# Performance work log

Measured on AMD Instinct MI355X. Metric: run time of the kernel, lower is better.

## Reference

```python
import jax, jax.numpy as jnp
import numpy as np

B, T, M, P = 256, 256, 512, 512


def setup_inputs() -> dict:
    key = jax.random.key(0)
    ks = jax.random.split(key, 10)
    sc = lambda fan: 1.0 / np.sqrt(fan)
    return {
        "H": jax.random.normal(ks[0], (B, T, M), jnp.float32),
        "d0": jax.random.normal(ks[1], (1, B, P), jnp.float32),
        "s0": jax.random.normal(ks[2], (1, B, P), jnp.float32),
        # TemporalAttention params (torch Linear convention: y = x @ W.T)
        "W_d": jax.random.uniform(ks[3], (M, 2 * P), jnp.float32, -sc(2 * P), sc(2 * P)),
        "U_d": jax.random.uniform(ks[4], (M, M), jnp.float32, -sc(M), sc(M)),
        "v_d": jax.random.uniform(ks[5], (1, M), jnp.float32, -sc(M), sc(M)),
        # LSTM params (torch nn.LSTM convention, gate order i,f,g,o)
        "W_ih": jax.random.uniform(ks[6], (4 * P, M), jnp.float32, -sc(P), sc(P)),
        "W_hh": jax.random.uniform(ks[7], (4 * P, P), jnp.float32, -sc(P), sc(P)),
        "b_ih": jax.random.uniform(ks[8], (4 * P,), jnp.float32, -sc(P), sc(P)),
        "b_hh": jax.random.uniform(ks[9], (4 * P,), jnp.float32, -sc(P), sc(P)),
    }


def reference(H, d0, s0, W_d, U_d, v_d, W_ih, W_hh, b_ih, b_hh):
    T_steps = H.shape[1]
    # U_d(H) is time-invariant across decode steps: precompute once. [B,T,m]
    UH = jnp.einsum("btm,nm->btn", H, U_d)
    v = v_d[0]  # [m]

    def step(carry, _):
        d, s = carry  # [B,p] hidden, [B,p] cell
        q = jnp.concatenate([d, s], axis=-1)            # [B,2p]
        wq = q @ W_d.T                                   # [B,m]
        e = jnp.tanh(wq[:, None, :] + UH) @ v            # [B,T]
        beta = jax.nn.softmax(e, axis=1)                 # softmax over time
        c_t = jnp.einsum("bt,btm->bm", beta, H)          # [B,m]
        gates = c_t @ W_ih.T + b_ih + d @ W_hh.T + b_hh  # [B,4p]
        i, f, g, o = jnp.split(gates, 4, axis=-1)
        s_new = jax.nn.sigmoid(f) * s + jax.nn.sigmoid(i) * jnp.tanh(g)
        d_new = jax.nn.sigmoid(o) * jnp.tanh(s_new)
        return (d_new, s_new), (beta, c_t)

    (d, s), (betas, cts) = jax.lax.scan(step, (d0[0], s0[0]), None, length=T_steps)
    attn = jnp.transpose(betas, (1, 0, 2))               # [B,T,T]
    out = jnp.concatenate([d[:, None, :], cts[-1][:, None, :]], axis=2)  # [B,1,p+m]
    return out, attn
```

## Files before the change

kernel.cpp:

```cpp
#include <hip/hip_runtime.h>
#include <hip/hip_fp16.h>

typedef _Float16 h4 __attribute__((ext_vector_type(4)));
typedef _Float16 h8 __attribute__((ext_vector_type(8)));
typedef float    f4 __attribute__((ext_vector_type(4)));

#define SC2LOG2E 2.8853900817779268f

__device__ __forceinline__ float v_exp2(float x) { float r; asm("v_exp_f32 %0, %1" : "=v"(r) : "v"(x)); return r; }
__device__ __forceinline__ float v_rcp (float x) { float r; asm("v_rcp_f32 %0, %1" : "=v"(r) : "v"(x)); return r; }
__device__ __forceinline__ float fast_tanh(float x) {
    float e = __expf(2.0f * x);
    return 1.0f - 2.0f * v_rcp(e + 1.0f);
}
__device__ __forceinline__ float fast_sigmoid(float x) {
    return v_rcp(1.0f + __expf(-x));
}

__device__ __forceinline__ h8 ld_h8_dc(const _Float16* p) {
    h8 r;
    asm volatile("global_load_dwordx4 %0, %1, off sc0 sc1" : "=v"(r) : "v"(p));
    return r;
}
__device__ __forceinline__ f4 ld_f4_dc(const float* p) {
    f4 r;
    asm volatile("global_load_dwordx4 %0, %1, off sc0 sc1" : "=v"(r) : "v"(p));
    return r;
}
__device__ __forceinline__ void st_f_dc(float* p, float v) {
    asm volatile("global_store_dword %0, %1, off sc0 sc1" :: "v"(p), "v"(v) : "memory");
}
__device__ __forceinline__ void st_h_dc(_Float16* p, _Float16 v) {
    unsigned u = (unsigned)__builtin_bit_cast(unsigned short, v);
    asm volatile("global_store_short %0, %1, off sc0 sc1" :: "v"(p), "v"(u) : "memory");
}

__global__ void convert_f16(const float* __restrict__ s, _Float16* __restrict__ d, int n) {
    int i = (blockIdx.x * 256 + threadIdx.x) * 4;
    if (i < n) {
        float4 v = *(const float4*)(s + i);
        h4 o = {(_Float16)v.x, (_Float16)v.y, (_Float16)v.z, (_Float16)v.w};
        *(h4*)(d + i) = o;
    }
}

__global__ void convert_cb(const float* __restrict__ H, _Float16* __restrict__ CB) {
    int i = (blockIdx.x * 256 + threadIdx.x) * 4;
    int r = i >> 9, m = i & 511;
    float4 v = *(const float4*)(H + i);
    h4 o = {(_Float16)v.x, (_Float16)v.y, (_Float16)v.z, (_Float16)v.w};
    *(h4*)(CB + (size_t)r * 1024 + 512 + m) = o;
}

__global__ void build_wg(const float* __restrict__ Wih, const float* __restrict__ Whh,
                         _Float16* __restrict__ Wg) {
    int idx = (blockIdx.x * 256 + threadIdx.x) * 4;
    int np = idx >> 10, k = idx & 1023;
    int p = np >> 2, g = np & 3, row = g * 512 + p;
    const float* src = (k < 512) ? Wih + (size_t)row * 512 + k
                                 : Whh + (size_t)row * 512 + (k - 512);
    float4 v = *(const float4*)src;
    h4 o = {(_Float16)v.x, (_Float16)v.y, (_Float16)v.z, (_Float16)v.w};
    *(h4*)(Wg + idx) = o;
}

__global__ void build_bsum(const float* __restrict__ bih, const float* __restrict__ bhh,
                           float* __restrict__ bsum) {
    int np = blockIdx.x * 256 + threadIdx.x;
    int p = np >> 2, g = np & 3, row = g * 512 + p;
    bsum[np] = bih[row] + bhh[row];
}

__global__ void init_state(const float* __restrict__ d0, const float* __restrict__ s0,
                           _Float16* __restrict__ qA, _Float16* __restrict__ ds) {
    int i = blockIdx.x * 256 + threadIdx.x;
    float dv = d0[i], sv = s0[i];
    int b = i >> 9, j = i & 511;
    qA[(size_t)b * 1024 + 512 + j] = (_Float16)dv;
    ds[(size_t)b * 1024 + j]       = (_Float16)dv;
    ds[(size_t)b * 1024 + 512 + j] = (_Float16)sv;
}

__global__ void zero_bar(unsigned* __restrict__ bar, int n) {
    int i = blockIdx.x * 256 + threadIdx.x;
    if (i < n) bar[i] = 0u;
}

__global__ __launch_bounds__(128) void uh_mfma(const float* __restrict__ H,
                                               const float* __restrict__ Ud,
                                               _Float16* __restrict__ CB) {
    int tid = threadIdx.x;
    int lane = tid & 63, w = tid >> 6;
    int ln = lane & 15, quad = lane >> 4;
    int m0 = blockIdx.x * 64, n0 = blockIdx.y * 32;
    f4 z = {0.f, 0.f, 0.f, 0.f};
    f4 acc[4] = {z, z, z, z};
    const float* brow = Ud + (size_t)(n0 + w * 16 + ln) * 512 + quad * 8;
    const float* arow = H  + (size_t)(m0 + ln) * 512 + quad * 8;
#pragma unroll 2
    for (int k = 0; k < 16; k++) {
        float4 bx = *(const float4*)(brow + k * 32);
        float4 by = *(const float4*)(brow + k * 32 + 4);
        h8 b = {(_Float16)bx.x, (_Float16)bx.y, (_Float16)bx.z, (_Float16)bx.w,
                (_Float16)by.x, (_Float16)by.y, (_Float16)by.z, (_Float16)by.w};
#pragma unroll
        for (int mt = 0; mt < 4; mt++) {
            const float* ap = arow + (size_t)mt * 16 * 512 + k * 32;
            float4 ax = *(const float4*)ap;
            float4 ay = *(const float4*)(ap + 4);
            h8 a = {(_Float16)ax.x, (_Float16)ax.y, (_Float16)ax.z, (_Float16)ax.w,
                    (_Float16)ay.x, (_Float16)ay.y, (_Float16)ay.z, (_Float16)ay.w};
            acc[mt] = __builtin_amdgcn_mfma_f32_16x16x32_f16(a, b, acc[mt], 0, 0, 0);
        }
    }
#pragma unroll
    for (int mt = 0; mt < 4; mt++)
#pragma unroll
        for (int r = 0; r < 4; r++)
            CB[(size_t)(m0 + mt * 16 + quad * 4 + r) * 1024 + n0 + w * 16 + ln] =
                (_Float16)(acc[mt][r] * SC2LOG2E);
}

__device__ __forceinline__ void gbar(unsigned* __restrict__ arrive,
                                     unsigned* __restrict__ gen,
                                     unsigned ticket) {
    __syncthreads();
    if (blockIdx.x == 0) {
        int tid = threadIdx.x;
        if (tid >= 1 && tid < 256) {
            while (__hip_atomic_load(arrive + (size_t)tid * 16, __ATOMIC_RELAXED,
                                     __HIP_MEMORY_SCOPE_AGENT) < ticket)
                __builtin_amdgcn_s_sleep(2);
        }
        __syncthreads();
        if (tid == 0)
            __hip_atomic_store(gen, ticket, __ATOMIC_RELAXED, __HIP_MEMORY_SCOPE_AGENT);
    } else {
        if (threadIdx.x == 0) {
            __hip_atomic_store(arrive + (size_t)blockIdx.x * 16, ticket,
                               __ATOMIC_RELAXED, __HIP_MEMORY_SCOPE_AGENT);
            while (__hip_atomic_load(gen, __ATOMIC_RELAXED,
                                     __HIP_MEMORY_SCOPE_AGENT) < ticket)
                __builtin_amdgcn_s_sleep(2);
        }
        __syncthreads();
    }
}

struct LoopArgs {
    const _Float16* CB;
    const _Float16* Wdh;
    const _Float16* Wg;
    const float*    bsum;
    const float*    vd;
    const float*    s0;
    float*          wq2;
    _Float16*       qA;
    _Float16*       qB;
    _Float16*       ds;
    float*          out;
    float*          attn;
    unsigned*       bar;
};

__global__ __launch_bounds__(1024) void decoder_loop(LoopArgs A) {
    const int bid = blockIdx.x;
    const int tid = threadIdx.x;
    const int lane = tid & 63, wv = tid >> 6;
    const int ln = lane & 15, quad = lane >> 4;

    __shared__ __align__(16) union {
        struct { float cpart[16][512]; float es2[256]; float m2s[16]; float zs[16]; } B;
        float gt[64][36];
    } sm;

    unsigned* arrive = A.bar;
    unsigned* gen    = A.bar + 4096;
    unsigned  bt     = 0;

    const int a_m0 = (bid >> 5) * 64, a_n0 = (bid & 31) * 16;
    const float4* vp = (const float4*)(A.vd + lane * 8);
    float4 vv0 = vp[0], vv1 = vp[1];
    float vr[8] = {vv0.x, vv0.y, vv0.z, vv0.w, vv1.x, vv1.y, vv1.z, vv1.w};
    const h8* ub0 = (const h8*)(A.CB + ((size_t)bid * 256 + wv * 16) * 1024) + lane;
    const int c_mt = wv & 3, c_nt = (wv >> 2) & 1;
    const int c_m0 = (bid & 3) * 64, c_by = bid >> 2;
    const int c_n0 = c_by * 32, c_p0 = c_by * 8;
    const float c_bs = A.bsum[c_n0 + c_nt * 16 + ln];
    const int c_ml = tid >> 3, c_pl = tid & 7;
    const int c_b = c_m0 + c_ml, c_p = c_p0 + c_pl;
    float s_state = (tid < 512) ? A.s0[(size_t)c_b * 512 + c_p] : 0.f;

#pragma unroll 1
    for (int t = 0; t < 256; ++t) {
        _Float16* qcur = (t & 1) ? A.qB : A.qA;
        _Float16* qnxt = (t & 1) ? A.qA : A.qB;

        if (bid < 128 && tid < 256) {
            f4 acc = {0.f, 0.f, 0.f, 0.f};
            const h8* ap = (const h8*)(A.ds  + (size_t)(a_m0 + wv * 16 + ln) * 1024) + quad;
            const h8* bp = (const h8*)(A.Wdh + (size_t)(a_n0 + ln) * 1024) + quad;
#pragma unroll
            for (int kc = 0; kc < 4; ++kc) {
                h8 areg[8];
#pragma unroll
                for (int u = 0; u < 8; ++u)
                    areg[u] = ld_h8_dc((const _Float16*)(ap + (kc * 8 + u) * 4));
                asm volatile("s_waitcnt vmcnt(0)" ::: "memory");
                __builtin_amdgcn_sched_barrier(0);
#pragma unroll
                for (int u = 0; u < 8; ++u)
                    acc = __builtin_amdgcn_mfma_f32_16x16x32_f16(areg[u], bp[(kc * 8 + u) * 4],
                                                                 acc, 0, 0, 0);
            }
#pragma unroll
            for (int r = 0; r < 4; ++r)
                st_f_dc(A.wq2 + (size_t)(a_m0 + wv * 16 + quad * 4 + r) * 512 + a_n0 + ln,
                        acc[r] * SC2LOG2E);
        }
        gbar(arrive, gen, ++bt);

        {
            f4 w0 = ld_f4_dc(A.wq2 + (size_t)bid * 512 + lane * 8);
            f4 w1 = ld_f4_dc(A.wq2 + (size_t)bid * 512 + lane * 8 + 4);
            asm volatile("s_waitcnt vmcnt(0)" ::: "memory");
            __builtin_amdgcn_sched_barrier(0);
            float wr[8] = {w0[0], w0[1], w0[2], w0[3], w1[0], w1[1], w1[2], w1[3]};

            float m2 = -1e30f, Z = 0.f;
            float ch[8] = {0.f, 0.f, 0.f, 0.f, 0.f, 0.f, 0.f, 0.f};
#pragma unroll 4
            for (int i = 0; i < 16; ++i) {
                h8 u  = ub0[(size_t)i * 128];
                h8 hv = ub0[(size_t)i * 128 + 64];
                float acc = 0.0f;
#pragma unroll
                for (int j = 0; j < 8; ++j) {
                    float zz = wr[j] + (float)u[j];
                    acc = fmaf(vr[j], v_rcp(1.0f + v_exp2(zz)), acc);
                }
#pragma unroll
                for (int o = 32; o; o >>= 1) acc += __shfl_xor(acc, o, 64);
                float e2 = -SC2LOG2E * acc;
                if (lane == 0) sm.B.es2[wv * 16 + i] = e2;
                if (e2 > m2) {
                    float s = v_exp2(m2 - e2);
                    Z *= s;
#pragma unroll
                    for (int k2 = 0; k2 < 8; ++k2) ch[k2] *= s;
                    m2 = e2;
                }
                float w = v_exp2(e2 - m2);
                Z += w;
#pragma unroll
                for (int k2 = 0; k2 < 8; ++k2) ch[k2] = fmaf(w, (float)hv[k2], ch[k2]);
            }
            *(float4*)&sm.B.cpart[wv][lane * 8]     = make_float4(ch[0], ch[1], ch[2], ch[3]);
            *(float4*)&sm.B.cpart[wv][lane * 8 + 4] = make_float4(ch[4], ch[5], ch[6], ch[7]);
            if (lane == 0) { sm.B.m2s[wv] = m2; sm.B.zs[wv] = Z; }
            __syncthreads();

            if (tid < 512) {
                float m2g = sm.B.m2s[0];
#pragma unroll
                for (int w2 = 1; w2 < 16; ++w2) m2g = fmaxf(m2g, sm.B.m2s[w2]);
                float Zg = 0.f, cg = 0.f;
#pragma unroll
                for (int w2 = 0; w2 < 16; ++w2) {
                    float f = v_exp2(sm.B.m2s[w2] - m2g);
                    Zg = fmaf(sm.B.zs[w2], f, Zg);
                    cg = fmaf(sm.B.cpart[w2][tid], f, cg);
                }
                float rz = v_rcp(Zg);
                float cval = cg * rz;
                st_h_dc(qcur + (size_t)bid * 1024 + tid, (_Float16)cval);
                if (t == 255) A.out[(size_t)bid * 1024 + 512 + tid] = cval;
                if (tid < 256) {
                    float beta = v_exp2(sm.B.es2[tid] - m2g) * rz;
                    __builtin_nontemporal_store(beta,
                        A.attn + (size_t)bid * 65536 + (size_t)t * 256 + tid);
                }
            }
        }
        gbar(arrive, gen, ++bt);

        {
            bool act = (tid < 512);
            if (act) {
                f4 acc = {0.f, 0.f, 0.f, 0.f};
                const h8* ap = (const h8*)(qcur + (size_t)(c_m0 + c_mt * 16 + ln) * 1024) + quad;
                const h8* bp = (const h8*)(A.Wg + (size_t)(c_n0 + c_nt * 16 + ln) * 1024) + quad;
#pragma unroll
                for (int kc = 0; kc < 4; ++kc) {
                    h8 areg[8];
#pragma unroll
                    for (int u = 0; u < 8; ++u)
                        areg[u] = ld_h8_dc((const _Float16*)(ap + (kc * 8 + u) * 4));
                    asm volatile("s_waitcnt vmcnt(0)" ::: "memory");
                    __builtin_amdgcn_sched_barrier(0);
#pragma unroll
                    for (int u = 0; u < 8; ++u)
                        acc = __builtin_amdgcn_mfma_f32_16x16x32_f16(areg[u], bp[(kc * 8 + u) * 4],
                                                                     acc, 0, 0, 0);
                }
#pragma unroll
                for (int r = 0; r < 4; ++r)
                    sm.gt[c_mt * 16 + quad * 4 + r][c_nt * 16 + ln] = acc[r] + c_bs;
            }
            __syncthreads();
            if (act) {
                float4 g4 = *(const float4*)&sm.gt[c_ml][c_pl * 4];
                float ig = fast_sigmoid(g4.x);
                float fg = fast_sigmoid(g4.y);
                float gg = fast_tanh(g4.z);
                float og = fast_sigmoid(g4.w);
                float snew = fmaf(fg, s_state, ig * gg);
                float dnew = og * fast_tanh(snew);
                s_state = snew;
                st_h_dc(qnxt + (size_t)c_b * 1024 + 512 + c_p, (_Float16)dnew);
                st_h_dc(A.ds + (size_t)c_b * 1024 + c_p,       (_Float16)dnew);
                st_h_dc(A.ds + (size_t)c_b * 1024 + 512 + c_p, (_Float16)snew);
                if (t == 255) A.out[(size_t)c_b * 1024 + c_p] = dnew;
            }
        }
        gbar(arrive, gen, ++bt);
    }
}

extern "C" void kernel_launch(void* const* d_in, const int* in_sizes, int n_in,
                              void* d_out, int out_size, void* d_ws, size_t ws_size,
                              hipStream_t stream) {
    const float* H   = (const float*)d_in[0];
    const float* d0  = (const float*)d_in[1];
    const float* s0  = (const float*)d_in[2];
    const float* Wd  = (const float*)d_in[3];
    const float* Ud  = (const float*)d_in[4];
    const float* vd  = (const float*)d_in[5];
    const float* Wih = (const float*)d_in[6];
    const float* Whh = (const float*)d_in[7];
    const float* bih = (const float*)d_in[8];
    const float* bhh = (const float*)d_in[9];

    float* out  = (float*)d_out;
    float* attn = out + 262144;

    char* ws = (char*)d_ws;
    size_t off = 0;
    _Float16* CB   = (_Float16*)(ws + off); off += 134217728;
    _Float16* Wdh  = (_Float16*)(ws + off); off += 1048576;
    _Float16* Wg   = (_Float16*)(ws + off); off += 4194304;
    float*    bsum = (float*)   (ws + off); off += 8192;
    float*    wq2  = (float*)   (ws + off); off += 524288;
    _Float16* qA   = (_Float16*)(ws + off); off += 524288;
    _Float16* qB   = (_Float16*)(ws + off); off += 524288;
    _Float16* ds   = (_Float16*)(ws + off); off += 524288;
    unsigned* bar  = (unsigned*)(ws + off); off += 32768;

    convert_f16<<<512, 256, 0, stream>>>(Wd, Wdh, 524288);
    build_wg<<<2048, 256, 0, stream>>>(Wih, Whh, Wg);
    build_bsum<<<8, 256, 0, stream>>>(bih, bhh, bsum);
    convert_cb<<<32768, 256, 0, stream>>>(H, CB);
    init_state<<<512, 256, 0, stream>>>(d0, s0, qA, ds);
    zero_bar<<<17, 256, 0, stream>>>(bar, 4097);
    uh_mfma<<<dim3(1024, 16), 128, 0, stream>>>(H, Ud, CB);

    LoopArgs la;
    la.CB = CB; la.Wdh = Wdh; la.Wg = Wg; la.bsum = bsum; la.vd = vd; la.s0 = s0;
    la.wq2 = wq2; la.qA = qA; la.qB = qB; la.ds = ds;
    la.out = out; la.attn = attn; la.bar = bar;
    void* kp[] = { &la };
    if (hipLaunchCooperativeKernel((void*)decoder_loop, dim3(256), dim3(1024),
                                   kp, 0, stream) != hipSuccess) {
        decoder_loop<<<dim3(256), dim3(1024), 0, stream>>>(la);
    }
}
```

Measured before the change: 16.22 ms.

## Halve decoder block size and prefetch attention UH/H rows across the barrier

Shrinks the persistent decoder kernel from 1024 to 512 threads per block, so each wave handles 32 time rows instead of 16. At the start of each step it issues register prefetches of the block's UH and H rows before the wq GEMM and grid barrier, then walks them with staged vmcnt waits, reissuing loads for the second half. The goal is to hide the global-memory latency of the attention scan behind the earlier phase and barrier, and to remove the idle half of the block in the gate phase. The cost is heavy register pressure from 32 held h8 vectors, which may cause spills, and fewer waves available to hide latency.

```diff
diff --git a/kernel.cpp b/kernel.cpp
--- a/kernel.cpp
+++ b/kernel.cpp
@@ -33,6 +33,31 @@
 __device__ __forceinline__ void st_h_dc(_Float16* p, _Float16 v) {
     unsigned u = (unsigned)__builtin_bit_cast(unsigned short, v);
     asm volatile("global_store_short %0, %1, off sc0 sc1" :: "v"(p), "v"(u) : "memory");
+}
+__device__ __forceinline__ h8 ld_h8(const _Float16* p) {
+    h8 r;
+    asm volatile("global_load_dwordx4 %0, %1, off" : "=v"(r) : "v"(p));
+    return r;
+}
+__device__ __forceinline__ void wait_vmcnt(int n) {
+    switch (n) {
+    case 0:  asm volatile("s_waitcnt vmcnt(0)"  ::: "memory"); break;
+    case 2:  asm volatile("s_waitcnt vmcnt(2)"  ::: "memory"); break;
+    case 4:  asm volatile("s_waitcnt vmcnt(4)"  ::: "memory"); break;
+    case 6:  asm volatile("s_waitcnt vmcnt(6)"  ::: "memory"); break;
+    case 8:  asm volatile("s_waitcnt vmcnt(8)"  ::: "memory"); break;
+    case 10: asm volatile("s_waitcnt vmcnt(10)" ::: "memory"); break;
+    case 12: asm volatile("s_waitcnt vmcnt(12)" ::: "memory"); break;
+    case 14: asm volatile("s_waitcnt vmcnt(14)" ::: "memory"); break;
+    case 16: asm volatile("s_waitcnt vmcnt(16)" ::: "memory"); break;
+    case 18: asm volatile("s_waitcnt vmcnt(18)" ::: "memory"); break;
+    case 20: asm volatile("s_waitcnt vmcnt(20)" ::: "memory"); break;
+    case 22: asm volatile("s_waitcnt vmcnt(22)" ::: "memory"); break;
+    case 24: asm volatile("s_waitcnt vmcnt(24)" ::: "memory"); break;
+    case 26: asm volatile("s_waitcnt vmcnt(26)" ::: "memory"); break;
+    case 28: asm volatile("s_waitcnt vmcnt(28)" ::: "memory"); break;
+    default: asm volatile("s_waitcnt vmcnt(30)" ::: "memory"); break;
+    }
 }
 
 __global__ void convert_f16(const float* __restrict__ s, _Float16* __restrict__ d, int n) {
@@ -163,14 +188,14 @@
     unsigned*       bar;
 };
 
-__global__ __launch_bounds__(1024) void decoder_loop(LoopArgs A) {
+__global__ __launch_bounds__(512, 2) void decoder_loop(LoopArgs A) {
     const int bid = blockIdx.x;
     const int tid = threadIdx.x;
     const int lane = tid & 63, wv = tid >> 6;
     const int ln = lane & 15, quad = lane >> 4;
 
     __shared__ __align__(16) union {
-        struct { float cpart[16][512]; float es2[256]; float m2s[16]; float zs[16]; } B;
+        struct { float cpart[8][512]; float es2[256]; float m2s[8]; float zs[8]; } B;
         float gt[64][36];
     } sm;
 
@@ -182,19 +207,26 @@
     const float4* vp = (const float4*)(A.vd + lane * 8);
     float4 vv0 = vp[0], vv1 = vp[1];
     float vr[8] = {vv0.x, vv0.y, vv0.z, vv0.w, vv1.x, vv1.y, vv1.z, vv1.w};
-    const h8* ub0 = (const h8*)(A.CB + ((size_t)bid * 256 + wv * 16) * 1024) + lane;
+    const _Float16* cb0 = A.CB + ((size_t)bid * 256 + wv * 32) * 1024 + lane * 8;
     const int c_mt = wv & 3, c_nt = (wv >> 2) & 1;
     const int c_m0 = (bid & 3) * 64, c_by = bid >> 2;
     const int c_n0 = c_by * 32, c_p0 = c_by * 8;
     const float c_bs = A.bsum[c_n0 + c_nt * 16 + ln];
     const int c_ml = tid >> 3, c_pl = tid & 7;
     const int c_b = c_m0 + c_ml, c_p = c_p0 + c_pl;
-    float s_state = (tid < 512) ? A.s0[(size_t)c_b * 512 + c_p] : 0.f;
+    float s_state = A.s0[(size_t)c_b * 512 + c_p];
 
 #pragma unroll 1
     for (int t = 0; t < 256; ++t) {
         _Float16* qcur = (t & 1) ? A.qB : A.qA;
         _Float16* qnxt = (t & 1) ? A.qA : A.qB;
+
+        h8 su[16], sh[16];
+#pragma unroll
+        for (int r = 0; r < 16; ++r) {
+            su[r] = ld_h8(cb0 + (size_t)r * 1024);
+            sh[r] = ld_h8(cb0 + (size_t)r * 1024 + 512);
+        }
 
         if (bid < 128 && tid < 256) {
             f4 acc = {0.f, 0.f, 0.f, 0.f};
@@ -229,10 +261,17 @@
 
             float m2 = -1e30f, Z = 0.f;
             float ch[8] = {0.f, 0.f, 0.f, 0.f, 0.f, 0.f, 0.f, 0.f};
-#pragma unroll 4
-            for (int i = 0; i < 16; ++i) {
-                h8 u  = ub0[(size_t)i * 128];
-                h8 hv = ub0[(size_t)i * 128 + 64];
+
+#pragma unroll
+            for (int r = 0; r < 32; ++r) {
+                wait_vmcnt(r < 16 ? 30 : 62 - 2 * r);
+                __builtin_amdgcn_sched_barrier(0);
+                h8 u  = su[r & 15];
+                h8 hv = sh[r & 15];
+                if (r < 16) {
+                    su[r & 15] = ld_h8(cb0 + (size_t)(r + 16) * 1024);
+                    sh[r & 15] = ld_h8(cb0 + (size_t)(r + 16) * 1024 + 512);
+                }
                 float acc = 0.0f;
 #pragma unroll
                 for (int j = 0; j < 8; ++j) {
@@ -242,7 +281,7 @@
 #pragma unroll
                 for (int o = 32; o; o >>= 1) acc += __shfl_xor(acc, o, 64);
                 float e2 = -SC2LOG2E * acc;
-                if (lane == 0) sm.B.es2[wv * 16 + i] = e2;
+                if (lane == 0) sm.B.es2[wv * 32 + r] = e2;
                 if (e2 > m2) {
                     float s = v_exp2(m2 - e2);
                     Z *= s;
@@ -260,13 +299,13 @@
             if (lane == 0) { sm.B.m2s[wv] = m2; sm.B.zs[wv] = Z; }
             __syncthreads();
 
-            if (tid < 512) {
+            {
                 float m2g = sm.B.m2s[0];
 #pragma unroll
-                for (int w2 = 1; w2 < 16; ++w2) m2g = fmaxf(m2g, sm.B.m2s[w2]);
+                for (int w2 = 1; w2 < 8; ++w2) m2g = fmaxf(m2g, sm.B.m2s[w2]);
                 float Zg = 0.f, cg = 0.f;
 #pragma unroll
-                for (int w2 = 0; w2 < 16; ++w2) {
+                for (int w2 = 0; w2 < 8; ++w2) {
                     float f = v_exp2(sm.B.m2s[w2] - m2g);
                     Zg = fmaf(sm.B.zs[w2], f, Zg);
                     cg = fmaf(sm.B.cpart[w2][tid], f, cg);
@@ -285,30 +324,27 @@
         gbar(arrive, gen, ++bt);
 
         {
-            bool act = (tid < 512);
-            if (act) {
-                f4 acc = {0.f, 0.f, 0.f, 0.f};
-                const h8* ap = (const h8*)(qcur + (size_t)(c_m0 + c_mt * 16 + ln) * 1024) + quad;
-                const h8* bp = (const h8*)(A.Wg + (size_t)(c_n0 + c_nt * 16 + ln) * 1024) + quad;
-#pragma unroll
-                for (int kc = 0; kc < 4; ++kc) {
-                    h8 areg[8];
-#pragma unroll
-                    for (int u = 0; u < 8; ++u)
-                        areg[u] = ld_h8_dc((const _Float16*)(ap + (kc * 8 + u) * 4));
-                    asm volatile("s_waitcnt vmcnt(0)" ::: "memory");
-                    __builtin_amdgcn_sched_barrier(0);
-#pragma unroll
-                    for (int u = 0; u < 8; ++u)
-                        acc = __builtin_amdgcn_mfma_f32_16x16x32_f16(areg[u], bp[(kc * 8 + u) * 4],
-                                                                     acc, 0, 0, 0);
-                }
-#pragma unroll
-                for (int r = 0; r < 4; ++r)
-                    sm.gt[c_mt * 16 + quad * 4 + r][c_nt * 16 + ln] = acc[r] + c_bs;
+            f4 acc = {0.f, 0.f, 0.f, 0.f};
+            const h8* ap = (const h8*)(qcur + (size_t)(c_m0 + c_mt * 16 + ln) * 1024) + quad;
+            const h8* bp = (const h8*)(A.Wg + (size_t)(c_n0 + c_nt * 16 + ln) * 1024) + quad;
+#pragma unroll
+            for (int kc = 0; kc < 4; ++kc) {
+                h8 areg[8];
+#pragma unroll
+                for (int u = 0; u < 8; ++u)
+                    areg[u] = ld_h8_dc((const _Float16*)(ap + (kc * 8 + u) * 4));
+                asm volatile("s_waitcnt vmcnt(0)" ::: "memory");
+                __builtin_amdgcn_sched_barrier(0);
+#pragma unroll
+                for (int u = 0; u < 8; ++u)
+                    acc = __builtin_amdgcn_mfma_f32_16x16x32_f16(areg[u], bp[(kc * 8 + u) * 4],
+                                                                 acc, 0, 0, 0);
             }
+#pragma unroll
+            for (int r = 0; r < 4; ++r)
+                sm.gt[c_mt * 16 + quad * 4 + r][c_nt * 16 + ln] = acc[r] + c_bs;
             __syncthreads();
-            if (act) {
+            {
                 float4 g4 = *(const float4*)&sm.gt[c_ml][c_pl * 4];
                 float ig = fast_sigmoid(g4.x);
                 float fg = fast_sigmoid(g4.y);
@@ -369,8 +405,8 @@
     la.wq2 = wq2; la.qA = qA; la.qB = qB; la.ds = ds;
     la.out = out; la.attn = attn; la.bar = bar;
     void* kp[] = { &la };
-    if (hipLaunchCooperativeKernel((void*)decoder_loop, dim3(256), dim3(1024),
+    if (hipLaunchCooperativeKernel((void*)decoder_loop, dim3(256), dim3(512),
                                    kp, 0, stream) != hipSuccess) {
-        decoder_loop<<<dim3(256), dim3(1024), 0, stream>>>(la);
-    }
-}
+        decoder_loop<<<dim3(256), dim3(512), 0, stream>>>(la);
+    }
+}
```

New measurement: 19.19 ms. 18.3% more time.
